# Kernel optimization log

Measured on AMD Instinct MI355X. Metric: run time of the kernel, lower is better.

## Reference

```python
import jax, jax.numpy as jnp
import numpy as np

IN_CH, OUT_CH, M1, M2 = 64, 64, 32, 32


def _powerlaw_psd_gaussian(key, exponent, n):
    """JAX port of colorednoise.powerlaw_psd_gaussian (fmin=0 default)."""
    f = jnp.fft.rfftfreq(n).astype(jnp.float32)  # [n//2+1]
    # fmin = max(0, 1/n); f[0]=0 is the only freq below it -> clamp to f[1]
    s_scale = jnp.where(f < 1.0 / n, f[1], f) ** (-exponent / 2.0)
    w = s_scale[1:]
    w = w.at[-1].multiply((1 + (n % 2)) / 2.0)  # Nyquist correction
    sigma = 2.0 * jnp.sqrt(jnp.sum(w * w)) / n
    kr, ki = jax.random.split(key)
    sr = jax.random.normal(kr, f.shape, jnp.float32) * s_scale
    si = jax.random.normal(ki, f.shape, jnp.float32) * s_scale
    if n % 2 == 0:
        si = si.at[-1].set(0.0)
        sr = sr.at[-1].multiply(jnp.sqrt(2.0))
    si = si.at[0].set(0.0)
    sr = sr.at[0].multiply(jnp.sqrt(2.0))
    return jnp.fft.irfft(sr + 1j * si, n=n) / sigma


def _compl_mul2d(t1, w, e_r, e_i, amp_r, amp_i, phi_r, phi_i, key):
    # Faithful to the torch code: stack over in-ch at dim=1 then sum dim=2
    # sums over the OUT channel axis => out[b,i,x,y] = t1[b,i,x,y]*sum_o w[i,o,x,y]
    out = t1 * jnp.sum(w, axis=1)[None]  # [B, IN_CH, M1, M2] complex
    b, c, m1, m2 = out.shape
    n = b * c * m1 * m2
    k1, k2 = jax.random.split(key)
    nr = jnp.roll(_powerlaw_psd_gaussian(k1, e_r, n), phi_r.astype(jnp.int32)) * amp_r
    ni = jnp.roll(_powerlaw_psd_gaussian(k2, e_i, n), phi_i.astype(jnp.int32)) * amp_i
    # original multiplies imag noise by amp_i twice (once in-place, once on reshape)
    noise = (nr + 1j * (ni * amp_i)).reshape(b, c, m1, m2)
    return out - noise


def _forward(x, w1, w2, exp_r, exp_i, nAmp_real, nAmp_imag, nPhase_real, nphase_imag):
    w1c = w1[..., 0] + 1j * w1[..., 1]  # [IN, OUT, M1, M2] complex64
    w2c = w2[..., 0] + 1j * w2[..., 1]
    e_r = jnp.median(exp_r)
    e_i = jnp.median(exp_i)
    amp_r = jnp.median(nAmp_real)
    amp_i = jnp.median(nAmp_imag)
    phi_r = jnp.median(nPhase_real)
    phi_i = jnp.median(nphase_imag)
    B, _, H, W = x.shape
    Wr = W // 2 + 1
    x_ft = jnp.fft.rfft2(x)  # [B, IN_CH, H, Wr]
    key = jax.random.key(42)
    kA, kB = jax.random.split(key)
    out_ft = jnp.zeros((B, OUT_CH, H, Wr), jnp.complex64)
    out_ft = out_ft.at[:, :, :M1, :M2].set(
        _compl_mul2d(x_ft[:, :, :M1, :M2], w1c, e_r, e_i, amp_r, amp_i, phi_r, phi_i, kA))
    out_ft = out_ft.at[:, :, -M1:, :M2].set(
        _compl_mul2d(x_ft[:, :, -M1:, :M2], w2c, e_r, e_i, amp_r, amp_i, phi_r, phi_i, kB))
    return jnp.fft.irfft2(out_ft, s=(H, W)).astype(jnp.float32)


def setup_inputs() -> dict:
    key = jax.random.key(0)
    ks = jax.random.split(key, 9)
    scale = 1.0 / (IN_CH * OUT_CH)
    return {
        "x": jax.random.normal(ks[0], (16, IN_CH, 256, 256), jnp.float32),
        "w1": scale * jax.random.uniform(ks[1], (IN_CH, OUT_CH, M1, M2, 2), jnp.float32),
        "w2": scale * jax.random.uniform(ks[2], (IN_CH, OUT_CH, M1, M2, 2), jnp.float32),
        "exp_r": jax.random.uniform(ks[3], (8,), jnp.float32),
        "exp_i": jax.random.uniform(ks[4], (8,), jnp.float32),
        "nAmp_real": jax.random.uniform(ks[5], (8,), jnp.float32),
        "nAmp_imag": jax.random.uniform(ks[6], (8,), jnp.float32),
        "nPhase_real": jax.random.normal(ks[7], (8,), jnp.float32),
        "nphase_imag": jax.random.normal(ks[8], (8,), jnp.float32),
    }


def reference(x, w1, w2, exp_r, exp_i, nAmp_real, nAmp_imag, nPhase_real, nphase_imag):
    return _forward(x, w1, w2, exp_r, exp_i, nAmp_real, nAmp_imag, nPhase_real, nphase_imag)
```

## Files before the change

kernel.cpp:

```cpp
#include <hip/hip_runtime.h>
#include <cstdint>

#define JPART 1
#define PART_XOR 1

constexpr uint32_t N20   = 1u << 20;
constexpr uint32_t NHALF = 1u << 19;
constexpr int SPT_STRIDE = 520;

struct Hdr {
  float e_r, e_i, amp_r, amp_i;
  int   phi_r, phi_i;
  float nhe_r, nhe_i;
  float scale_s[4];
};
struct KeyArgs { uint32_t k[8][2]; };

typedef __attribute__((ext_vector_type(8))) short short8;
typedef __attribute__((ext_vector_type(16))) float f32x16;

__device__ inline f32x16 zero16() {
  f32x16 v;
  #pragma unroll
  for (int i = 0; i < 16; ++i) v[i] = 0.f;
  return v;
}

__device__ inline unsigned short f2bf(float f) {
  uint32_t u = __float_as_uint(f);
  return (unsigned short)((u + 0x7fffu + ((u >> 16) & 1u)) >> 16);
}

__host__ __device__ inline void tf2x32(uint32_t k0, uint32_t k1, uint32_t x0, uint32_t x1,
                                       uint32_t& o0, uint32_t& o1) {
  const uint32_t ks0 = k0, ks1 = k1, ks2 = k0 ^ k1 ^ 0x1BD11BDAu;
  const uint32_t ks[3] = { ks0, ks1, ks2 };
  x0 += ks0; x1 += ks1;
  const int rot[2][4] = { {13,15,26,6}, {17,29,16,24} };
  for (int g = 0; g < 5; ++g) {
    const int* rr = rot[g & 1];
    for (int i = 0; i < 4; ++i) {
      x0 += x1;
      x1 = (x1 << rr[i]) | (x1 >> (32 - rr[i]));
      x1 ^= x0;
    }
    x0 += ks[(g + 1) % 3];
    x1 += ks[(g + 2) % 3] + (uint32_t)(g + 1);
  }
  o0 = x0; o1 = x1;
}

__device__ inline float erfinv_xla(float x) {
  float w = -log1pf(-x * x);
  float p;
  if (w < 5.0f) {
    w -= 2.5f;
    p = 2.81022636e-08f;
    p = fmaf(p, w, 3.43273939e-07f);
    p = fmaf(p, w, -3.5233877e-06f);
    p = fmaf(p, w, -4.39150654e-06f);
    p = fmaf(p, w, 0.00021858087f);
    p = fmaf(p, w, -0.00125372503f);
    p = fmaf(p, w, -0.00417768164f);
    p = fmaf(p, w, 0.246640727f);
    p = fmaf(p, w, 1.50140941f);
  } else {
    w = sqrtf(w) - 3.0f;
    p = -0.000200214257f;
    p = fmaf(p, w, 0.000100950558f);
    p = fmaf(p, w, 0.00134934322f);
    p = fmaf(p, w, -0.00367342844f);
    p = fmaf(p, w, 0.00573950773f);
    p = fmaf(p, w, -0.0076224613f);
    p = fmaf(p, w, 0.00943887047f);
    p = fmaf(p, w, 1.00167406f);
    p = fmaf(p, w, 2.83297682f);
  }
  return p * x;
}

__device__ inline float normal_from_bits(uint32_t bits) {
  uint32_t fb = (bits >> 9) | 0x3f800000u;
  float f = __uint_as_float(fb) - 1.0f;
  const float LO = -0.99999994f;
  float u = f * 2.0f + LO;
  u = fmaxf(LO, u);
  return 1.41421356f * erfinv_xla(u);
}

__device__ inline float sscale_f(uint32_t k, float nhe) {
  uint32_t kk = k ? k : 1u;
  return powf((float)kk * (1.0f / 1048576.0f), nhe);
}

__device__ inline float2 cmul(float2 a, float2 b) {
  return make_float2(a.x * b.x - a.y * b.y, a.x * b.y + a.y * b.x);
}
__device__ inline float2 wexp(float u) {
  float s, c; sincospif(2.0f * u, &s, &c); return make_float2(c, s);
}
__device__ inline float2 cadd(float2 a, float2 b){ return make_float2(a.x+b.x, a.y+b.y); }
__device__ inline float2 csub(float2 a, float2 b){ return make_float2(a.x-b.x, a.y-b.y); }
__device__ inline float2 cmuli(float2 a){ return make_float2(-a.y, a.x); }

__device__ inline int sA(int p) { return p ^ (((p >> 6) & 3) << 2) ^ ((p >> 8) & 3); }

__device__ inline void bfly(float2& y0, float2& y1, float2& y2, float2& y3, float2 W) {
  float2 a = cadd(y0, y2), b = csub(y0, y2);
  float2 c = cadd(y1, y3), d = cmuli(csub(y1, y3));
  float2 W2 = cmul(W, W), W3 = cmul(W2, W);
  y0 = cadd(a, c);
  y1 = cmul(cadd(b, d), W);
  y2 = cmul(csub(a, c), W2);
  y3 = cmul(csub(b, d), W3);
}

__device__ inline void fft1024_core(float2* r, float2* rc, float2* buf, int w) {
  #pragma unroll
  for (int e3 = 0; e3 < 4; ++e3) {
    float2 W = wexp((float)((e3 << 6) + w) * (1.0f / 1024.0f));
    bfly(r[e3], r[e3 + 4], r[e3 + 8], r[e3 + 12], W);
  }
  {
    float2 W = wexp((float)w * (1.0f / 256.0f));
    #pragma unroll
    for (int e4 = 0; e4 < 4; ++e4)
      bfly(r[(e4 << 2) + 0], r[(e4 << 2) + 1], r[(e4 << 2) + 2], r[(e4 << 2) + 3], W);
  }
  #pragma unroll
  for (int s = 0; s < 16; ++s) buf[sA((s << 6) + w)] = r[s];
  __syncthreads();
  {
    const int e0 = w & 3;
    const int pbase = ((w >> 4) << 8) + (((w >> 2) & 3) << 6) + e0;
    float2 rb[16];
    #pragma unroll
    for (int e2 = 0; e2 < 4; ++e2)
      #pragma unroll
      for (int e1 = 0; e1 < 4; ++e1)
        rb[(e2 << 2) + e1] = buf[sA(pbase + (e2 << 4) + (e1 << 2))];
    #pragma unroll
    for (int e1 = 0; e1 < 4; ++e1) {
      float2 W = wexp((float)((e1 << 2) + e0) * (1.0f / 64.0f));
      bfly(rb[e1], rb[e1 + 4], rb[e1 + 8], rb[e1 + 12], W);
    }
    {
      float2 W = wexp((float)e0 * (1.0f / 16.0f));
      #pragma unroll
      for (int e2 = 0; e2 < 4; ++e2)
        bfly(rb[(e2 << 2) + 0], rb[(e2 << 2) + 1], rb[(e2 << 2) + 2], rb[(e2 << 2) + 3], W);
    }
    #pragma unroll
    for (int e2 = 0; e2 < 4; ++e2)
      #pragma unroll
      for (int e1 = 0; e1 < 4; ++e1)
        buf[sA(pbase + (e2 << 4) + (e1 << 2))] = rb[(e2 << 2) + e1];
  }
  __syncthreads();
  {
    const int cbase = ((w >> 4) << 8) + (((w >> 2) & 3) << 6) + ((w & 3) << 4);
    #pragma unroll
    for (int e1 = 0; e1 < 4; ++e1)
      #pragma unroll
      for (int e0 = 0; e0 < 4; ++e0)
        rc[(e1 << 2) + e0] = buf[sA(cbase + (e1 << 2) + e0)];
    #pragma unroll
    for (int e1 = 0; e1 < 4; ++e1) {
      float2 x0 = rc[(e1 << 2)], x1 = rc[(e1 << 2) + 1], x2 = rc[(e1 << 2) + 2], x3 = rc[(e1 << 2) + 3];
      float2 a = cadd(x0, x2), b = csub(x0, x2);
      float2 c = cadd(x1, x3), d = cmuli(csub(x1, x3));
      rc[(e1 << 2)]     = cadd(a, c);
      rc[(e1 << 2) + 1] = cadd(b, d);
      rc[(e1 << 2) + 2] = csub(a, c);
      rc[(e1 << 2) + 3] = csub(b, d);
    }
  }
}

__device__ inline float med8_dev(const float* p) {
  float v[8];
  for (int i = 0; i < 8; ++i) v[i] = p[i];
  for (int i = 1; i < 8; ++i) { float key = v[i]; int j = i - 1;
    while (j >= 0 && v[j] > key) { v[j + 1] = v[j]; --j; } v[j + 1] = key; }
  return 0.5f * (v[3] + v[4]);
}

__global__ void k_scalars(Hdr* h, const float* er, const float* ei, const float* ar,
                          const float* ai, const float* pr, const float* pim) {
  if (threadIdx.x || blockIdx.x) return;
  float mer = med8_dev(er), mei = med8_dev(ei);
  h->e_r = mer; h->e_i = mei;
  h->amp_r = med8_dev(ar); h->amp_i = med8_dev(ai);
  h->phi_r = (int)med8_dev(pr);
  h->phi_i = (int)med8_dev(pim);
  h->nhe_r = -0.5f * mer; h->nhe_i = -0.5f * mei;
}

__global__ void k_sumw2(const Hdr* __restrict__ h, float* __restrict__ partials) {
  __shared__ float sr_[256], si_[256];
  const float nher = h->nhe_r, nhei = h->nhe_i;
  float sr = 0.f, si = 0.f;
  for (int j = 0; j < 4; ++j) {
    uint32_t k = (uint32_t)(blockIdx.x * 1024 + j * 256 + threadIdx.x) + 1u;
    float fk = (float)k * (1.0f / 1048576.0f);
    float wr = powf(fk, nher), wi = powf(fk, nhei);
    if (k == NHALF) { wr *= 0.5f; wi *= 0.5f; }
    sr += wr * wr; si += wi * wi;
  }
  sr_[threadIdx.x] = sr; si_[threadIdx.x] = si; __syncthreads();
  for (int off = 128; off > 0; off >>= 1) {
    if ((int)threadIdx.x < off) { sr_[threadIdx.x] += sr_[threadIdx.x + off];
                                  si_[threadIdx.x] += si_[threadIdx.x + off]; }
    __syncthreads();
  }
  if (!threadIdx.x) { partials[blockIdx.x * 2] = sr_[0]; partials[blockIdx.x * 2 + 1] = si_[0]; }
}

__global__ void k_sumw2_fin(Hdr* h, const float* partials) {
  if (threadIdx.x || blockIdx.x) return;
  float Sr = 0.f, Si = 0.f;
  for (int b = 0; b < 512; ++b) { Sr += partials[b * 2]; Si += partials[b * 2 + 1]; }
  float sig_r = 2.0f * sqrtf(Sr) * (1.0f / 1048576.0f);
  float sig_i = 2.0f * sqrtf(Si) * (1.0f / 1048576.0f);
  float s0 = h->amp_r / (sig_r * 1048576.0f);
  float s1 = (h->amp_i * h->amp_i) / (sig_i * 1048576.0f);
  h->scale_s[0] = s0; h->scale_s[1] = s1; h->scale_s[2] = s0; h->scale_s[3] = s1;
}

__global__ void k_wsum(const float* __restrict__ w1, const float* __restrict__ w2,
                       float2* __restrict__ wsum) {
  int idx = blockIdx.x * 256 + threadIdx.x;
  int sel = idx >> 16, rem = idx & 65535;
  const float* w = sel ? w2 : w1;
  int c = rem >> 10, m1 = (rem >> 5) & 31, m2 = rem & 31;
  size_t base = (size_t)c * 131072 + (size_t)m1 * 64 + (size_t)m2 * 2;
  float sr = 0.f, si = 0.f;
  for (int oc = 0; oc < 64; ++oc) { sr += w[base + (size_t)oc * 2048]; si += w[base + (size_t)oc * 2048 + 1]; }
  wsum[idx] = make_float2(sr, si);
}

__global__ void k_noise_spec(float4* __restrict__ spT, const Hdr* __restrict__ h, KeyArgs ka) {
  const int pair = blockIdx.y;
  const int bx = blockIdx.x;
  const int k1 = bx >> 1, chunk = bx & 1;
  const int k2 = (chunk << 8) + (int)threadIdx.x;
  const float nher = h->nhe_r, nhei = h->nhe_i;
  float4* row = spT + (size_t)pair * (1024 * SPT_STRIDE) + (size_t)k1 * SPT_STRIDE;
  const bool extra = (k1 == 0) && (chunk == 1) && (threadIdx.x == 255);
  const int niter = extra ? 2 : 1;
  for (int it = 0; it < niter; ++it) {
    const int kk2 = (it == 0) ? k2 : 512;
    const uint32_t i = (uint32_t)k1 + ((uint32_t)kk2 << 10);
    float vals[4];
    #pragma unroll
    for (int j = 0; j < 4; ++j) {
      const uint32_t K0 = ka.k[pair * 4 + j][0], K1 = ka.k[pair * 4 + j][1];
      uint32_t o0, o1; tf2x32(K0, K1, 0u, i, o0, o1);
#if PART_XOR
      uint32_t bits = o0 ^ o1;
#else
      uint32_t bits = o1;
#endif
      float nhe = (j < 2) ? nher : nhei;
      float v = normal_from_bits(bits) * sscale_f(i, nhe);
      if (i == 0u || i == NHALF) v = (j & 1) ? 0.0f : v * 1.41421356f;
      vals[j] = v;
    }
    row[kk2] = make_float4(vals[0], vals[1], vals[2], vals[3]);
  }
}

__global__ __launch_bounds__(256) void k_fft_s1(const float4* __restrict__ spT,
                                                float2* __restrict__ G) {
  __shared__ float2 buf4[4][1024];
  const int b = blockIdx.x;
  const int lin = (b & 7) * 64 + (b >> 3);
  const int pair = lin >> 8;
  const int g = threadIdx.x >> 6, w = threadIdx.x & 63;
  const int k1 = ((lin & 255) << 2) + g;
  const float4* sp = spT + (size_t)pair * (1024 * SPT_STRIDE);
  const int mrow = (1024 - k1) & 1023;

  float2 r[16], rc[16];
  #pragma unroll
  for (int s = 0; s < 16; ++s) {
    int k2 = (s << 6) + w;
    uint32_t k = (uint32_t)k1 + ((uint32_t)k2 << 10);
    float4 f; float2 z;
    if (k <= NHALF) {
      f = sp[(size_t)k1 * SPT_STRIDE + k2];
      z = make_float2(f.x - f.w, f.y + f.z);
    } else {
      int k2p = (k1 == 0) ? (1024 - k2) : (1023 - k2);
      f = sp[(size_t)mrow * SPT_STRIDE + k2p];
      z = make_float2(f.x + f.w, f.z - f.y);
    }
    r[s] = z;
  }
  fft1024_core(r, rc, buf4[g], w);
  float2* gp = G + ((size_t)pair << 20) + ((size_t)k1 << 10);
  const int klo = ((w & 3) << 4) + (((w >> 2) & 3) << 2) + (w >> 4);
  #pragma unroll
  for (int e1 = 0; e1 < 4; ++e1)
    #pragma unroll
    for (int e0 = 0; e0 < 4; ++e0) {
      int k = (e0 << 8) + (e1 << 6) + klo;
      float2 tw = wexp((float)(k * k1) * (1.0f / 1048576.0f));
      gp[k] = cmul(rc[(e1 << 2) + e0], tw);
    }
}

__global__ __launch_bounds__(256) void k_fft_s2(const float2* __restrict__ G,
                                                float2* __restrict__ noiseP,
                                                const Hdr* __restrict__ h) {
  __shared__ float2 buf4[4][1024];
  const int b = blockIdx.x;
  const int lin = (b & 7) * 64 + (b >> 3);
  const int pair = lin >> 8;
  const int g = threadIdx.x >> 6, w = threadIdx.x & 63;
  const int j2 = ((lin & 255) << 2) + g;

  float2 r[16], rc[16];
  const float2* gp = G + ((size_t)pair << 20) + (size_t)j2;
  #pragma unroll
  for (int s = 0; s < 16; ++s) r[s] = gp[(size_t)((s << 6) + w) << 10];
  fft1024_core(r, rc, buf4[g], w);
  const float scr = h->scale_s[0], sci = h->scale_s[1];
  float2* np_ = noiseP + ((size_t)pair << 20) + ((size_t)j2 << 10);
  const int klo = ((w & 3) << 4) + (((w >> 2) & 3) << 2) + (w >> 4);
  #pragma unroll
  for (int e1 = 0; e1 < 4; ++e1)
    #pragma unroll
    for (int e0 = 0; e0 < 4; ++e0) {
      int k = (e0 << 8) + (e1 << 6) + klo;
      np_[k] = make_float2(rc[(e1 << 2) + e0].x * scr, rc[(e1 << 2) + e0].y * sci);
    }
}

__global__ __launch_bounds__(256) void k_ntrans(const float2* __restrict__ noiseP,
                                                float* __restrict__ noiseL,
                                                const Hdr* __restrict__ h) {
  __shared__ float tr[64][65];
  __shared__ float ti[64][65];
  const int b = blockIdx.x;
  const int pair = b >> 8, tid = b & 255;
  const int R0 = (tid >> 4) << 6;
  const int C0 = (tid & 15) << 6;
  const int t = threadIdx.x;
  const int tx = t & 63, ty = t >> 6;
  const int phir = h->phi_r, phii = h->phi_i;
  const float2* src = noiseP + ((size_t)pair << 20);
  float* dstr = noiseL + ((size_t)(pair * 2) << 20);
  float* dsti = noiseL + ((size_t)(pair * 2 + 1) << 20);
  #pragma unroll
  for (int i = 0; i < 16; ++i) {
    int r = (i << 2) + ty;
    float2 v = src[(size_t)((R0 + r) << 10) + (size_t)(C0 + tx)];
    tr[r][tx] = v.x; ti[r][tx] = v.y;
  }
  __syncthreads();
  #pragma unroll
  for (int i = 0; i < 16; ++i) {
    int c = (i << 2) + ty;
    int n = ((C0 + c) << 10) + R0 + tx;
    dstr[(uint32_t)(n + phir) & (N20 - 1u)] = tr[tx][c];
    dsti[(uint32_t)(n + phii) & (N20 - 1u)] = ti[tx][c];
  }
}

__global__ __launch_bounds__(256) void k_prep(unsigned short* __restrict__ A_E,
                                              unsigned short* __restrict__ B2T,
                                              unsigned short* __restrict__ ET,
                                              unsigned short* __restrict__ Fc,
                                              unsigned short* __restrict__ Fs,
                                              unsigned short* __restrict__ Fns) {
  int t = blockIdx.x * 256 + threadIdx.x;
  if (t < 32768) {
    int y = t >> 7, p = t & 127;
    int kyp = p & 63; int ky = (kyp < 32) ? kyp : kyp + 192;
    float s, c; sincospif(2.0f * (float)((ky * y) & 255) * (1.0f / 256.0f), &s, &c);
    A_E[t] = f2bf((p < 64) ? c : s);
  } else if (t < 49152) {
    int u = t - 32768;
    int x = u >> 6, j = u & 63, kx = j & 31;
    float s, c; sincospif(2.0f * (float)((kx * x) & 255) * (1.0f / 256.0f), &s, &c);
    float v = (j < 32) ? ((kx == 0) ? 1.0f : 2.0f * c)
                       : ((kx == 0) ? 0.0f : -2.0f * s);
    B2T[u] = f2bf(v * (1.0f / 65536.0f));
  } else if (t < 65536) {
    int u = t - 49152;
    int col = u >> 8, xx = u & 255; int kx = col & 31;
    float s, c; sincospif(2.0f * (float)((kx * xx) & 255) * (1.0f / 256.0f), &s, &c);
    ET[u] = f2bf((col < 32) ? c : -s);
  } else if (t < 114688) {
    int u = (t - 65536) & 16383;
    int which = (t - 65536) >> 14;
    int kyp = u >> 8, y = u & 255; int ky = (kyp < 32) ? kyp : kyp + 192;
    float s, c; sincospif(2.0f * (float)((ky * y) & 255) * (1.0f / 256.0f), &s, &c);
    if (which == 0) Fc[u] = f2bf(c);
    else if (which == 1) Fs[u] = f2bf(s);
    else Fns[u] = f2bf(-s);
  }
}

__global__ __launch_bounds__(256, 2) void k_forward(const float* __restrict__ x,
    const float2* __restrict__ wsum, const float* __restrict__ noiseL,
    const unsigned short* __restrict__ ET, const unsigned short* __restrict__ Fc,
    const unsigned short* __restrict__ Fs, const unsigned short* __restrict__ Fns,
    float2* __restrict__ oftg) {
  __shared__ char lds[65536];
  char* X1T = lds + 32768;
  const int bc = blockIdx.x, t = threadIdx.x;
  const int c = bc & 63;
  const int l = t & 63, w = t >> 6, lr = l & 31, kg = l >> 5;
  const int rt = w >> 1, ct = w & 1;
  const float* xim = x + ((size_t)bc << 16);

  const int r_  = t >> 2;
  (void)r_;
  float4 pf[16];
  #pragma unroll
  for (int i = 0; i < 16; ++i) {
    int f4 = i * 256 + t;
    int r = f4 >> 6, c4 = f4 & 63;
    pf[i] = *(const float4*)(xim + (size_t)((r) << 8) + (c4 << 2));
  }

  #pragma unroll
  for (int yt = 0; yt < 4; ++yt) {
    __syncthreads();
    #pragma unroll
    for (int i = 0; i < 16; ++i) {
      int f4 = i * 256 + t;
      int r = f4 >> 6, c4 = f4 & 63;
      ushort4 b4; b4.x = f2bf(pf[i].x); b4.y = f2bf(pf[i].y);
      b4.z = f2bf(pf[i].z); b4.w = f2bf(pf[i].w);
      int byte = ((r << 9) + (c4 << 3)) ^ ((r & 7) << 4);
      *(ushort4*)(lds + byte) = b4;
    }
    __syncthreads();
    if (yt < 3) {
      #pragma unroll
      for (int i = 0; i < 16; ++i) {
        int f4 = i * 256 + t;
        int r = f4 >> 6, c4 = f4 & 63;
        pf[i] = *(const float4*)(xim + (size_t)((((yt + 1) << 6) + r) << 8) + (c4 << 2));
      }
    }
    f32x16 a1 = zero16();
    const int arow = (rt << 5) + lr;
    const int bcol = (ct << 5) + lr;
    #pragma unroll
    for (int s = 0; s < 16; ++s) {
      short8 af = *(const short8*)(lds + (((arow << 9) + (s << 5) + (kg << 4)) ^ ((arow & 7) << 4)));
      short8 bf = *(const short8*)(ET + (bcol << 8) + (s << 4) + (kg << 3));
      a1 = __builtin_amdgcn_mfma_f32_32x32x16_bf16(af, bf, a1, 0, 0, 0);
    }
    #pragma unroll
    for (int r4 = 0; r4 < 4; ++r4) {
      int y0 = (yt << 6) + (rt << 5) + (r4 << 3) + (kg << 2);
      ushort4 p4;
      p4.x = f2bf(a1[r4 * 4 + 0]); p4.y = f2bf(a1[r4 * 4 + 1]);
      p4.z = f2bf(a1[r4 * 4 + 2]); p4.w = f2bf(a1[r4 * 4 + 3]);
      int byte = ((bcol << 9) + (y0 << 1)) ^ ((bcol & 7) << 4);
      *(ushort4*)(X1T + byte) = p4;
    }
  }
  __syncthreads();

  const int re_im = w >> 1, kt = w & 1;
  const unsigned short* A1p = re_im ? Fns : Fs;
  const int b0row = (re_im ? 32 : 0) + lr;
  const int b1row = (re_im ? 0 : 32) + lr;
  const int a2row = (kt << 5) + lr;
  f32x16 a2 = zero16();
  #pragma unroll
  for (int s = 0; s < 16; ++s) {
    short8 a0f = *(const short8*)(Fc  + (a2row << 8) + (s << 4) + (kg << 3));
    short8 a1f = *(const short8*)(A1p + (a2row << 8) + (s << 4) + (kg << 3));
    short8 b0f = *(const short8*)(X1T + (((b0row << 9) + (s << 5) + (kg << 4)) ^ ((b0row & 7) << 4)));
    short8 b1f = *(const short8*)(X1T + (((b1row << 9) + (s << 5) + (kg << 4)) ^ ((b1row & 7) << 4)));
    a2 = __builtin_amdgcn_mfma_f32_32x32x16_bf16(a0f, b0f, a2, 0, 0, 0);
    a2 = __builtin_amdgcn_mfma_f32_32x32x16_bf16(a1f, b1f, a2, 0, 0, 0);
  }
  float* Osm = (float*)(lds + (re_im << 13));
  #pragma unroll
  for (int i = 0; i < 16; ++i) {
    int row = (kt << 5) + (i & 3) + ((i >> 2) << 3) + (kg << 2);
    Osm[(row << 5) + lr] = a2[i];
  }
  __syncthreads();

  const float* Ore = (const float*)lds;
  const float* Oim = (const float*)(lds + 8192);
  #pragma unroll
  for (int r = 0; r < 8; ++r) {
    int idx = (r << 8) + t;
    int kyp = idx >> 5, kx = idx & 31;
    int sel = kyp >> 5, m1 = kyp & 31;
    float2 av = make_float2(Ore[idx], Oim[idx]);
    float2 wv = wsum[((size_t)sel << 16) + (size_t)(((c << 5) | m1) << 5) + (size_t)kx];
    float2 v;
    v.x = av.x * wv.x - av.y * wv.y;
    v.y = av.x * wv.y + av.y * wv.x;
    uint32_t p = ((uint32_t)((bc << 5) | m1) << 5) | (uint32_t)kx;
    const float* nlr = noiseL + ((size_t)(sel ? 2 : 0) << 20);
    const float* nli = noiseL + ((size_t)(sel ? 3 : 1) << 20);
    v.x -= nlr[p];
    v.y -= nli[p];
    oftg[((size_t)bc << 11) + (size_t)idx] = v;
  }
}

__global__ __launch_bounds__(256) void k_inverse(const float2* __restrict__ oftg,
    const unsigned short* __restrict__ A_E, const unsigned short* __restrict__ B2T,
    float* __restrict__ out) {
  __shared__ char smem[49152];
  char* Tb = smem + 16384;
  float* ofs = (float*)(smem + 16384);

  const int bc = blockIdx.x, t = threadIdx.x;
  const int l = t & 63, w = t >> 6, lr = l & 31, kg = l >> 5;

  {
    const float4* src = (const float4*)(oftg + ((size_t)bc << 11));
    float4* dst = (float4*)ofs;
    #pragma unroll
    for (int i = 0; i < 4; ++i) dst[t + (i << 8)] = src[t + (i << 8)];
  }
  __syncthreads();

  #pragma unroll
  for (int i = 0; i < 32; ++i) {
    int idx = t + (i << 8);
    int p = idx >> 6, j = idx & 63;
    int kyp = p & 63;
    float v;
    if (p < 64) v = (j < 32) ? ofs[(kyp << 6) + (j << 1)]
                             : ofs[(kyp << 6) + ((j - 32) << 1) + 1];
    else        v = (j < 32) ? -ofs[(kyp << 6) + (j << 1) + 1]
                             : ofs[(kyp << 6) + ((j - 32) << 1)];
    int byte = ((j << 8) + (p << 1)) ^ ((j & 7) << 4);
    *(unsigned short*)(smem + byte) = f2bf(v);
  }
  __syncthreads();

  f32x16 acc[2][2];
  acc[0][0] = zero16(); acc[0][1] = zero16(); acc[1][0] = zero16(); acc[1][1] = zero16();
  #pragma unroll
  for (int s = 0; s < 8; ++s) {
    short8 af[2], bf[2];
    #pragma unroll
    for (int rt = 0; rt < 2; ++rt) {
      int row = (w << 6) + (rt << 5) + lr;
      af[rt] = *(const short8*)(A_E + (row << 7) + (s << 4) + (kg << 3));
    }
    #pragma unroll
    for (int ct = 0; ct < 2; ++ct) {
      int j = (ct << 5) + lr;
      int byte = ((j << 8) + (s << 5) + (kg << 4)) ^ ((j & 7) << 4);
      bf[ct] = *(const short8*)(smem + byte);
    }
    #pragma unroll
    for (int rt = 0; rt < 2; ++rt)
      #pragma unroll
      for (int ct = 0; ct < 2; ++ct)
        acc[rt][ct] = __builtin_amdgcn_mfma_f32_32x32x16_bf16(af[rt], bf[ct], acc[rt][ct], 0, 0, 0);
  }

  #pragma unroll
  for (int rt = 0; rt < 2; ++rt)
    #pragma unroll
    for (int ct = 0; ct < 2; ++ct)
      #pragma unroll
      for (int r = 0; r < 16; ++r) {
        int row = (w << 6) + (rt << 5) + (r & 3) + (((r >> 2) & 3) << 3) + (kg << 2);
        int col = (ct << 5) + lr;
        int byte = ((row << 7) + (col << 1)) ^ ((row & 7) << 4);
        *(unsigned short*)(Tb + byte) = f2bf(acc[rt][ct][r]);
      }
  __syncthreads();

  short8 ta[2][4];
  #pragma unroll
  for (int rt = 0; rt < 2; ++rt)
    #pragma unroll
    for (int ks = 0; ks < 4; ++ks) {
      int row = (w << 6) + (rt << 5) + lr;
      int byte = ((row << 7) + (ks << 5) + (kg << 4)) ^ ((row & 7) << 4);
      ta[rt][ks] = *(const short8*)(Tb + byte);
    }
  float* op = out + ((size_t)bc << 16);
  #pragma unroll
  for (int cc = 0; cc < 4; ++cc) {
    short8 b2[2][4];
    #pragma unroll
    for (int cx = 0; cx < 2; ++cx)
      #pragma unroll
      for (int ks = 0; ks < 4; ++ks) {
        int xx = (cc << 6) + (cx << 5) + lr;
        b2[cx][ks] = *(const short8*)(B2T + (xx << 6) + (ks << 4) + (kg << 3));
      }
    f32x16 a2[2][2];
    a2[0][0] = zero16(); a2[0][1] = zero16(); a2[1][0] = zero16(); a2[1][1] = zero16();
    #pragma unroll
    for (int ks = 0; ks < 4; ++ks)
      #pragma unroll
      for (int rt = 0; rt < 2; ++rt)
        #pragma unroll
        for (int cx = 0; cx < 2; ++cx)
          a2[rt][cx] = __builtin_amdgcn_mfma_f32_32x32x16_bf16(ta[rt][ks], b2[cx][ks], a2[rt][cx], 0, 0, 0);
    #pragma unroll
    for (int rt = 0; rt < 2; ++rt)
      #pragma unroll
      for (int cx = 0; cx < 2; ++cx)
        #pragma unroll
        for (int r = 0; r < 16; ++r) {
          int row = (w << 6) + (rt << 5) + (r & 3) + (((r >> 2) & 3) << 3) + (kg << 2);
          int xx = (cc << 6) + (cx << 5) + lr;
          op[(row << 8) + xx] = a2[rt][cx][r];
        }
  }
}

extern "C" void kernel_launch(void* const* d_in, const int* in_sizes, int n_in,
                              void* d_out, int out_size, void* d_ws, size_t ws_size,
                              hipStream_t stream) {
  (void)in_sizes; (void)n_in; (void)out_size; (void)ws_size;
  const float* x   = (const float*)d_in[0];
  const float* w1  = (const float*)d_in[1];
  const float* w2  = (const float*)d_in[2];
  const float* er  = (const float*)d_in[3];
  const float* ei  = (const float*)d_in[4];
  const float* ar  = (const float*)d_in[5];
  const float* ai  = (const float*)d_in[6];
  const float* pr  = (const float*)d_in[7];
  const float* pim = (const float*)d_in[8];
  float* out = (float*)d_out;

  char* ws = (char*)d_ws;
  Hdr*    hdr      = (Hdr*)ws;
  float*  partials = (float*)(ws + 0x1000);
  float2* wsum     = (float2*)(ws + 0x10000);
  unsigned short* A_E = (unsigned short*)(ws + 0x130000);
  unsigned short* B2T = (unsigned short*)(ws + 0x140000);
  unsigned short* ET  = (unsigned short*)(ws + 0x148000);
  unsigned short* Fc  = (unsigned short*)(ws + 0x150000);
  unsigned short* Fs  = (unsigned short*)(ws + 0x158000);
  unsigned short* Fns = (unsigned short*)(ws + 0x160000);
  float4* spT      = (float4*)(ws + 0x200000);
  float2* G        = (float2*)(ws + 0x1400000);
  float2* oft      = (float2*)(ws + 0x1400000);
  float2* noiseP   = (float2*)(ws + 0x2400000);
  float*  noiseL   = (float*)(ws + 0x3400000);

  auto splitk = [](const uint32_t k[2], uint32_t a[2], uint32_t b[2]) {
#if JPART
    tf2x32(k[0], k[1], 0u, 0u, a[0], a[1]);
    tf2x32(k[0], k[1], 0u, 1u, b[0], b[1]);
#else
    uint32_t r0[2], r1[2];
    tf2x32(k[0], k[1], 0u, 2u, r0[0], r0[1]);
    tf2x32(k[0], k[1], 1u, 3u, r1[0], r1[1]);
    a[0] = r0[0]; a[1] = r1[0]; b[0] = r0[1]; b[1] = r1[1];
#endif
  };
  uint32_t root[2] = { 0u, 42u };
  uint32_t kA[2], kB[2], k1A[2], k2A[2], k1B[2], k2B[2];
  splitk(root, kA, kB);
  splitk(kA, k1A, k2A);
  splitk(kB, k1B, k2B);
  KeyArgs ka;
  splitk(k1A, ka.k[0], ka.k[1]);
  splitk(k2A, ka.k[2], ka.k[3]);
  splitk(k1B, ka.k[4], ka.k[5]);
  splitk(k2B, ka.k[6], ka.k[7]);

  hipLaunchKernelGGL(k_scalars,    dim3(1),        dim3(64),  0, stream, hdr, er, ei, ar, ai, pr, pim);
  hipLaunchKernelGGL(k_sumw2,      dim3(512),      dim3(256), 0, stream, hdr, partials);
  hipLaunchKernelGGL(k_sumw2_fin,  dim3(1),        dim3(64),  0, stream, hdr, partials);
  hipLaunchKernelGGL(k_wsum,       dim3(512),      dim3(256), 0, stream, w1, w2, wsum);
  hipLaunchKernelGGL(k_prep,       dim3(448),      dim3(256), 0, stream, A_E, B2T, ET, Fc, Fs, Fns);
  hipLaunchKernelGGL(k_noise_spec, dim3(2048, 2),  dim3(256), 0, stream, spT, hdr, ka);
  hipLaunchKernelGGL(k_fft_s1,     dim3(512),      dim3(256), 0, stream, spT, G);
  hipLaunchKernelGGL(k_fft_s2,     dim3(512),      dim3(256), 0, stream, G, noiseP, hdr);
  hipLaunchKernelGGL(k_ntrans,     dim3(512),      dim3(256), 0, stream, noiseP, noiseL, hdr);
  hipLaunchKernelGGL(k_forward,    dim3(1024),     dim3(256), 0, stream, x, wsum, noiseL, ET, Fc, Fs, Fns, oft);
  hipLaunchKernelGGL(k_inverse,    dim3(1024),     dim3(256), 0, stream, oft, A_E, B2T, out);
}
```

Measured before the change: 270.7 us.

## Merge small setup kernels into combined launches and shrink inverse-kernel shared memory

Folds the scalar medians, weight summation and basis prep into one k_misc launch, and the sum-of-squares reduction plus noise spectrum generation into one k_gen launch. This cuts the launch count from eleven to eight and lets independent small jobs share the GPU. k_inverse now reads oft straight from global memory instead of staging it in LDS, and reuses one 32KB buffer with an extra barrier. The aim is lower launch overhead and higher occupancy from the smaller LDS footprint, at the cost of uncoalesced global gathers in k_inverse.

After: 267.8 us. Within noise of the previous version (-1.1%).

```diff
diff --git a/kernel.cpp b/kernel.cpp
--- a/kernel.cpp
+++ b/kernel.cpp
@@ -185,196 +185,37 @@
   return 0.5f * (v[3] + v[4]);
 }
 
-__global__ void k_scalars(Hdr* h, const float* er, const float* ei, const float* ar,
-                          const float* ai, const float* pr, const float* pim) {
-  if (threadIdx.x || blockIdx.x) return;
-  float mer = med8_dev(er), mei = med8_dev(ei);
-  h->e_r = mer; h->e_i = mei;
-  h->amp_r = med8_dev(ar); h->amp_i = med8_dev(ai);
-  h->phi_r = (int)med8_dev(pr);
-  h->phi_i = (int)med8_dev(pim);
-  h->nhe_r = -0.5f * mer; h->nhe_i = -0.5f * mei;
-}
-
-__global__ void k_sumw2(const Hdr* __restrict__ h, float* __restrict__ partials) {
-  __shared__ float sr_[256], si_[256];
-  const float nher = h->nhe_r, nhei = h->nhe_i;
-  float sr = 0.f, si = 0.f;
-  for (int j = 0; j < 4; ++j) {
-    uint32_t k = (uint32_t)(blockIdx.x * 1024 + j * 256 + threadIdx.x) + 1u;
-    float fk = (float)k * (1.0f / 1048576.0f);
-    float wr = powf(fk, nher), wi = powf(fk, nhei);
-    if (k == NHALF) { wr *= 0.5f; wi *= 0.5f; }
-    sr += wr * wr; si += wi * wi;
-  }
-  sr_[threadIdx.x] = sr; si_[threadIdx.x] = si; __syncthreads();
-  for (int off = 128; off > 0; off >>= 1) {
-    if ((int)threadIdx.x < off) { sr_[threadIdx.x] += sr_[threadIdx.x + off];
-                                  si_[threadIdx.x] += si_[threadIdx.x + off]; }
-    __syncthreads();
-  }
-  if (!threadIdx.x) { partials[blockIdx.x * 2] = sr_[0]; partials[blockIdx.x * 2 + 1] = si_[0]; }
-}
-
-__global__ void k_sumw2_fin(Hdr* h, const float* partials) {
-  if (threadIdx.x || blockIdx.x) return;
-  float Sr = 0.f, Si = 0.f;
-  for (int b = 0; b < 512; ++b) { Sr += partials[b * 2]; Si += partials[b * 2 + 1]; }
-  float sig_r = 2.0f * sqrtf(Sr) * (1.0f / 1048576.0f);
-  float sig_i = 2.0f * sqrtf(Si) * (1.0f / 1048576.0f);
-  float s0 = h->amp_r / (sig_r * 1048576.0f);
-  float s1 = (h->amp_i * h->amp_i) / (sig_i * 1048576.0f);
-  h->scale_s[0] = s0; h->scale_s[1] = s1; h->scale_s[2] = s0; h->scale_s[3] = s1;
-}
-
-__global__ void k_wsum(const float* __restrict__ w1, const float* __restrict__ w2,
-                       float2* __restrict__ wsum) {
-  int idx = blockIdx.x * 256 + threadIdx.x;
-  int sel = idx >> 16, rem = idx & 65535;
-  const float* w = sel ? w2 : w1;
-  int c = rem >> 10, m1 = (rem >> 5) & 31, m2 = rem & 31;
-  size_t base = (size_t)c * 131072 + (size_t)m1 * 64 + (size_t)m2 * 2;
-  float sr = 0.f, si = 0.f;
-  for (int oc = 0; oc < 64; ++oc) { sr += w[base + (size_t)oc * 2048]; si += w[base + (size_t)oc * 2048 + 1]; }
-  wsum[idx] = make_float2(sr, si);
-}
-
-__global__ void k_noise_spec(float4* __restrict__ spT, const Hdr* __restrict__ h, KeyArgs ka) {
-  const int pair = blockIdx.y;
-  const int bx = blockIdx.x;
-  const int k1 = bx >> 1, chunk = bx & 1;
-  const int k2 = (chunk << 8) + (int)threadIdx.x;
-  const float nher = h->nhe_r, nhei = h->nhe_i;
-  float4* row = spT + (size_t)pair * (1024 * SPT_STRIDE) + (size_t)k1 * SPT_STRIDE;
-  const bool extra = (k1 == 0) && (chunk == 1) && (threadIdx.x == 255);
-  const int niter = extra ? 2 : 1;
-  for (int it = 0; it < niter; ++it) {
-    const int kk2 = (it == 0) ? k2 : 512;
-    const uint32_t i = (uint32_t)k1 + ((uint32_t)kk2 << 10);
-    float vals[4];
-    #pragma unroll
-    for (int j = 0; j < 4; ++j) {
-      const uint32_t K0 = ka.k[pair * 4 + j][0], K1 = ka.k[pair * 4 + j][1];
-      uint32_t o0, o1; tf2x32(K0, K1, 0u, i, o0, o1);
-#if PART_XOR
-      uint32_t bits = o0 ^ o1;
-#else
-      uint32_t bits = o1;
-#endif
-      float nhe = (j < 2) ? nher : nhei;
-      float v = normal_from_bits(bits) * sscale_f(i, nhe);
-      if (i == 0u || i == NHALF) v = (j & 1) ? 0.0f : v * 1.41421356f;
-      vals[j] = v;
-    }
-    row[kk2] = make_float4(vals[0], vals[1], vals[2], vals[3]);
-  }
-}
-
-__global__ __launch_bounds__(256) void k_fft_s1(const float4* __restrict__ spT,
-                                                float2* __restrict__ G) {
-  __shared__ float2 buf4[4][1024];
+__global__ __launch_bounds__(256) void k_misc(Hdr* h,
+    const float* er, const float* ei, const float* ar, const float* ai,
+    const float* pr, const float* pim,
+    const float* __restrict__ w1, const float* __restrict__ w2,
+    float2* __restrict__ wsum,
+    unsigned short* __restrict__ A_E, unsigned short* __restrict__ B2T,
+    unsigned short* __restrict__ ET, unsigned short* __restrict__ Fc,
+    unsigned short* __restrict__ Fs, unsigned short* __restrict__ Fns) {
   const int b = blockIdx.x;
-  const int lin = (b & 7) * 64 + (b >> 3);
-  const int pair = lin >> 8;
-  const int g = threadIdx.x >> 6, w = threadIdx.x & 63;
-  const int k1 = ((lin & 255) << 2) + g;
-  const float4* sp = spT + (size_t)pair * (1024 * SPT_STRIDE);
-  const int mrow = (1024 - k1) & 1023;
-
-  float2 r[16], rc[16];
-  #pragma unroll
-  for (int s = 0; s < 16; ++s) {
-    int k2 = (s << 6) + w;
-    uint32_t k = (uint32_t)k1 + ((uint32_t)k2 << 10);
-    float4 f; float2 z;
-    if (k <= NHALF) {
-      f = sp[(size_t)k1 * SPT_STRIDE + k2];
-      z = make_float2(f.x - f.w, f.y + f.z);
-    } else {
-      int k2p = (k1 == 0) ? (1024 - k2) : (1023 - k2);
-      f = sp[(size_t)mrow * SPT_STRIDE + k2p];
-      z = make_float2(f.x + f.w, f.z - f.y);
-    }
-    r[s] = z;
-  }
-  fft1024_core(r, rc, buf4[g], w);
-  float2* gp = G + ((size_t)pair << 20) + ((size_t)k1 << 10);
-  const int klo = ((w & 3) << 4) + (((w >> 2) & 3) << 2) + (w >> 4);
-  #pragma unroll
-  for (int e1 = 0; e1 < 4; ++e1)
-    #pragma unroll
-    for (int e0 = 0; e0 < 4; ++e0) {
-      int k = (e0 << 8) + (e1 << 6) + klo;
-      float2 tw = wexp((float)(k * k1) * (1.0f / 1048576.0f));
-      gp[k] = cmul(rc[(e1 << 2) + e0], tw);
-    }
-}
-
-__global__ __launch_bounds__(256) void k_fft_s2(const float2* __restrict__ G,
-                                                float2* __restrict__ noiseP,
-                                                const Hdr* __restrict__ h) {
-  __shared__ float2 buf4[4][1024];
-  const int b = blockIdx.x;
-  const int lin = (b & 7) * 64 + (b >> 3);
-  const int pair = lin >> 8;
-  const int g = threadIdx.x >> 6, w = threadIdx.x & 63;
-  const int j2 = ((lin & 255) << 2) + g;
-
-  float2 r[16], rc[16];
-  const float2* gp = G + ((size_t)pair << 20) + (size_t)j2;
-  #pragma unroll
-  for (int s = 0; s < 16; ++s) r[s] = gp[(size_t)((s << 6) + w) << 10];
-  fft1024_core(r, rc, buf4[g], w);
-  const float scr = h->scale_s[0], sci = h->scale_s[1];
-  float2* np_ = noiseP + ((size_t)pair << 20) + ((size_t)j2 << 10);
-  const int klo = ((w & 3) << 4) + (((w >> 2) & 3) << 2) + (w >> 4);
-  #pragma unroll
-  for (int e1 = 0; e1 < 4; ++e1)
-    #pragma unroll
-    for (int e0 = 0; e0 < 4; ++e0) {
-      int k = (e0 << 8) + (e1 << 6) + klo;
-      np_[k] = make_float2(rc[(e1 << 2) + e0].x * scr, rc[(e1 << 2) + e0].y * sci);
-    }
-}
-
-__global__ __launch_bounds__(256) void k_ntrans(const float2* __restrict__ noiseP,
-                                                float* __restrict__ noiseL,
-                                                const Hdr* __restrict__ h) {
-  __shared__ float tr[64][65];
-  __shared__ float ti[64][65];
-  const int b = blockIdx.x;
-  const int pair = b >> 8, tid = b & 255;
-  const int R0 = (tid >> 4) << 6;
-  const int C0 = (tid & 15) << 6;
-  const int t = threadIdx.x;
-  const int tx = t & 63, ty = t >> 6;
-  const int phir = h->phi_r, phii = h->phi_i;
-  const float2* src = noiseP + ((size_t)pair << 20);
-  float* dstr = noiseL + ((size_t)(pair * 2) << 20);
-  float* dsti = noiseL + ((size_t)(pair * 2 + 1) << 20);
-  #pragma unroll
-  for (int i = 0; i < 16; ++i) {
-    int r = (i << 2) + ty;
-    float2 v = src[(size_t)((R0 + r) << 10) + (size_t)(C0 + tx)];
-    tr[r][tx] = v.x; ti[r][tx] = v.y;
-  }
-  __syncthreads();
-  #pragma unroll
-  for (int i = 0; i < 16; ++i) {
-    int c = (i << 2) + ty;
-    int n = ((C0 + c) << 10) + R0 + tx;
-    dstr[(uint32_t)(n + phir) & (N20 - 1u)] = tr[tx][c];
-    dsti[(uint32_t)(n + phii) & (N20 - 1u)] = ti[tx][c];
-  }
-}
-
-__global__ __launch_bounds__(256) void k_prep(unsigned short* __restrict__ A_E,
-                                              unsigned short* __restrict__ B2T,
-                                              unsigned short* __restrict__ ET,
-                                              unsigned short* __restrict__ Fc,
-                                              unsigned short* __restrict__ Fs,
-                                              unsigned short* __restrict__ Fns) {
-  int t = blockIdx.x * 256 + threadIdx.x;
+  if (b == 960) {
+    if (threadIdx.x) return;
+    float mer = med8_dev(er), mei = med8_dev(ei);
+    h->e_r = mer; h->e_i = mei;
+    h->amp_r = med8_dev(ar); h->amp_i = med8_dev(ai);
+    h->phi_r = (int)med8_dev(pr);
+    h->phi_i = (int)med8_dev(pim);
+    h->nhe_r = -0.5f * mer; h->nhe_i = -0.5f * mei;
+    return;
+  }
+  if (b < 512) {
+    int idx = b * 256 + threadIdx.x;
+    int sel = idx >> 16, rem = idx & 65535;
+    const float* w = sel ? w2 : w1;
+    int c = rem >> 10, m1 = (rem >> 5) & 31, m2 = rem & 31;
+    size_t base = (size_t)c * 131072 + (size_t)m1 * 64 + (size_t)m2 * 2;
+    float sr = 0.f, si = 0.f;
+    for (int oc = 0; oc < 64; ++oc) { sr += w[base + (size_t)oc * 2048]; si += w[base + (size_t)oc * 2048 + 1]; }
+    wsum[idx] = make_float2(sr, si);
+    return;
+  }
+  int t = (b - 512) * 256 + threadIdx.x;
   if (t < 32768) {
     int y = t >> 7, p = t & 127;
     int kyp = p & 63; int ky = (kyp < 32) ? kyp : kyp + 192;
@@ -403,6 +244,170 @@
   }
 }
 
+__global__ __launch_bounds__(256) void k_gen(const Hdr* __restrict__ h,
+                                             float* __restrict__ partials,
+                                             float4* __restrict__ spT, KeyArgs ka) {
+  __shared__ float sr_[256], si_[256];
+  const int b = blockIdx.x;
+  if (b < 512) {
+    const float nher = h->nhe_r, nhei = h->nhe_i;
+    float sr = 0.f, si = 0.f;
+    for (int j = 0; j < 4; ++j) {
+      uint32_t k = (uint32_t)(b * 1024 + j * 256 + threadIdx.x) + 1u;
+      float fk = (float)k * (1.0f / 1048576.0f);
+      float wr = powf(fk, nher), wi = powf(fk, nhei);
+      if (k == NHALF) { wr *= 0.5f; wi *= 0.5f; }
+      sr += wr * wr; si += wi * wi;
+    }
+    sr_[threadIdx.x] = sr; si_[threadIdx.x] = si; __syncthreads();
+    for (int off = 128; off > 0; off >>= 1) {
+      if ((int)threadIdx.x < off) { sr_[threadIdx.x] += sr_[threadIdx.x + off];
+                                    si_[threadIdx.x] += si_[threadIdx.x + off]; }
+      __syncthreads();
+    }
+    if (!threadIdx.x) { partials[b * 2] = sr_[0]; partials[b * 2 + 1] = si_[0]; }
+    return;
+  }
+  const int idx = b - 512;
+  const int pair = idx >> 11;
+  const int bx = idx & 2047;
+  const int k1 = bx >> 1, chunk = bx & 1;
+  const int k2 = (chunk << 8) + (int)threadIdx.x;
+  const float nher = h->nhe_r, nhei = h->nhe_i;
+  float4* row = spT + (size_t)pair * (1024 * SPT_STRIDE) + (size_t)k1 * SPT_STRIDE;
+  const bool extra = (k1 == 0) && (chunk == 1) && (threadIdx.x == 255);
+  const int niter = extra ? 2 : 1;
+  for (int it = 0; it < niter; ++it) {
+    const int kk2 = (it == 0) ? k2 : 512;
+    const uint32_t i = (uint32_t)k1 + ((uint32_t)kk2 << 10);
+    float vals[4];
+    #pragma unroll
+    for (int j = 0; j < 4; ++j) {
+      const uint32_t K0 = ka.k[pair * 4 + j][0], K1 = ka.k[pair * 4 + j][1];
+      uint32_t o0, o1; tf2x32(K0, K1, 0u, i, o0, o1);
+#if PART_XOR
+      uint32_t bits = o0 ^ o1;
+#else
+      uint32_t bits = o1;
+#endif
+      float nhe = (j < 2) ? nher : nhei;
+      float v = normal_from_bits(bits) * sscale_f(i, nhe);
+      if (i == 0u || i == NHALF) v = (j & 1) ? 0.0f : v * 1.41421356f;
+      vals[j] = v;
+    }
+    row[kk2] = make_float4(vals[0], vals[1], vals[2], vals[3]);
+  }
+}
+
+__global__ void k_sumw2_fin(Hdr* h, const float* partials) {
+  if (threadIdx.x || blockIdx.x) return;
+  float Sr = 0.f, Si = 0.f;
+  for (int b = 0; b < 512; ++b) { Sr += partials[b * 2]; Si += partials[b * 2 + 1]; }
+  float sig_r = 2.0f * sqrtf(Sr) * (1.0f / 1048576.0f);
+  float sig_i = 2.0f * sqrtf(Si) * (1.0f / 1048576.0f);
+  float s0 = h->amp_r / (sig_r * 1048576.0f);
+  float s1 = (h->amp_i * h->amp_i) / (sig_i * 1048576.0f);
+  h->scale_s[0] = s0; h->scale_s[1] = s1; h->scale_s[2] = s0; h->scale_s[3] = s1;
+}
+
+__global__ __launch_bounds__(256) void k_fft_s1(const float4* __restrict__ spT,
+                                                float2* __restrict__ G) {
+  __shared__ float2 buf4[4][1024];
+  const int b = blockIdx.x;
+  const int lin = (b & 7) * 64 + (b >> 3);
+  const int pair = lin >> 8;
+  const int g = threadIdx.x >> 6, w = threadIdx.x & 63;
+  const int k1 = ((lin & 255) << 2) + g;
+  const float4* sp = spT + (size_t)pair * (1024 * SPT_STRIDE);
+  const int mrow = (1024 - k1) & 1023;
+
+  float2 r[16], rc[16];
+  #pragma unroll
+  for (int s = 0; s < 16; ++s) {
+    int k2 = (s << 6) + w;
+    uint32_t k = (uint32_t)k1 + ((uint32_t)k2 << 10);
+    float4 f; float2 z;
+    if (k <= NHALF) {
+      f = sp[(size_t)k1 * SPT_STRIDE + k2];
+      z = make_float2(f.x - f.w, f.y + f.z);
+    } else {
+      int k2p = (k1 == 0) ? (1024 - k2) : (1023 - k2);
+      f = sp[(size_t)mrow * SPT_STRIDE + k2p];
+      z = make_float2(f.x + f.w, f.z - f.y);
+    }
+    r[s] = z;
+  }
+  fft1024_core(r, rc, buf4[g], w);
+  float2* gp = G + ((size_t)pair << 20) + ((size_t)k1 << 10);
+  const int klo = ((w & 3) << 4) + (((w >> 2) & 3) << 2) + (w >> 4);
+  #pragma unroll
+  for (int e1 = 0; e1 < 4; ++e1)
+    #pragma unroll
+    for (int e0 = 0; e0 < 4; ++e0) {
+      int k = (e0 << 8) + (e1 << 6) + klo;
+      float2 tw = wexp((float)(k * k1) * (1.0f / 1048576.0f));
+      gp[k] = cmul(rc[(e1 << 2) + e0], tw);
+    }
+}
+
+__global__ __launch_bounds__(256) void k_fft_s2(const float2* __restrict__ G,
+                                                float2* __restrict__ noiseP,
+                                                const Hdr* __restrict__ h) {
+  __shared__ float2 buf4[4][1024];
+  const int b = blockIdx.x;
+  const int lin = (b & 7) * 64 + (b >> 3);
+  const int pair = lin >> 8;
+  const int g = threadIdx.x >> 6, w = threadIdx.x & 63;
+  const int j2 = ((lin & 255) << 2) + g;
+
+  float2 r[16], rc[16];
+  const float2* gp = G + ((size_t)pair << 20) + (size_t)j2;
+  #pragma unroll
+  for (int s = 0; s < 16; ++s) r[s] = gp[(size_t)((s << 6) + w) << 10];
+  fft1024_core(r, rc, buf4[g], w);
+  const float scr = h->scale_s[0], sci = h->scale_s[1];
+  float2* np_ = noiseP + ((size_t)pair << 20) + ((size_t)j2 << 10);
+  const int klo = ((w & 3) << 4) + (((w >> 2) & 3) << 2) + (w >> 4);
+  #pragma unroll
+  for (int e1 = 0; e1 < 4; ++e1)
+    #pragma unroll
+    for (int e0 = 0; e0 < 4; ++e0) {
+      int k = (e0 << 8) + (e1 << 6) + klo;
+      np_[k] = make_float2(rc[(e1 << 2) + e0].x * scr, rc[(e1 << 2) + e0].y * sci);
+    }
+}
+
+__global__ __launch_bounds__(256) void k_ntrans(const float2* __restrict__ noiseP,
+                                                float* __restrict__ noiseL,
+                                                const Hdr* __restrict__ h) {
+  __shared__ float tr[64][65];
+  __shared__ float ti[64][65];
+  const int b = blockIdx.x;
+  const int pair = b >> 8, tid = b & 255;
+  const int R0 = (tid >> 4) << 6;
+  const int C0 = (tid & 15) << 6;
+  const int t = threadIdx.x;
+  const int tx = t & 63, ty = t >> 6;
+  const int phir = h->phi_r, phii = h->phi_i;
+  const float2* src = noiseP + ((size_t)pair << 20);
+  float* dstr = noiseL + ((size_t)(pair * 2) << 20);
+  float* dsti = noiseL + ((size_t)(pair * 2 + 1) << 20);
+  #pragma unroll
+  for (int i = 0; i < 16; ++i) {
+    int r = (i << 2) + ty;
+    float2 v = src[(size_t)((R0 + r) << 10) + (size_t)(C0 + tx)];
+    tr[r][tx] = v.x; ti[r][tx] = v.y;
+  }
+  __syncthreads();
+  #pragma unroll
+  for (int i = 0; i < 16; ++i) {
+    int c = (i << 2) + ty;
+    int n = ((C0 + c) << 10) + R0 + tx;
+    dstr[(uint32_t)(n + phir) & (N20 - 1u)] = tr[tx][c];
+    dsti[(uint32_t)(n + phii) & (N20 - 1u)] = ti[tx][c];
+  }
+}
+
 __global__ __launch_bounds__(256, 2) void k_forward(const float* __restrict__ x,
     const float2* __restrict__ wsum, const float* __restrict__ noiseL,
     const unsigned short* __restrict__ ET, const unsigned short* __restrict__ Fc,
@@ -416,8 +421,6 @@
   const int rt = w >> 1, ct = w & 1;
   const float* xim = x + ((size_t)bc << 16);
 
-  const int r_  = t >> 2;
-  (void)r_;
   float4 pf[16];
   #pragma unroll
   for (int i = 0; i < 16; ++i) {
@@ -515,33 +518,26 @@
 __global__ __launch_bounds__(256) void k_inverse(const float2* __restrict__ oftg,
     const unsigned short* __restrict__ A_E, const unsigned short* __restrict__ B2T,
     float* __restrict__ out) {
-  __shared__ char smem[49152];
-  char* Tb = smem + 16384;
-  float* ofs = (float*)(smem + 16384);
+  __shared__ char smem[32768];
 
   const int bc = blockIdx.x, t = threadIdx.x;
   const int l = t & 63, w = t >> 6, lr = l & 31, kg = l >> 5;
 
   {
-    const float4* src = (const float4*)(oftg + ((size_t)bc << 11));
-    float4* dst = (float4*)ofs;
-    #pragma unroll
-    for (int i = 0; i < 4; ++i) dst[t + (i << 8)] = src[t + (i << 8)];
-  }
-  __syncthreads();
-
-  #pragma unroll
-  for (int i = 0; i < 32; ++i) {
-    int idx = t + (i << 8);
-    int p = idx >> 6, j = idx & 63;
-    int kyp = p & 63;
-    float v;
-    if (p < 64) v = (j < 32) ? ofs[(kyp << 6) + (j << 1)]
-                             : ofs[(kyp << 6) + ((j - 32) << 1) + 1];
-    else        v = (j < 32) ? -ofs[(kyp << 6) + (j << 1) + 1]
-                             : ofs[(kyp << 6) + ((j - 32) << 1)];
-    int byte = ((j << 8) + (p << 1)) ^ ((j & 7) << 4);
-    *(unsigned short*)(smem + byte) = f2bf(v);
+    const float* ob = (const float*)(oftg + ((size_t)bc << 11));
+    #pragma unroll
+    for (int i = 0; i < 32; ++i) {
+      int idx = t + (i << 8);
+      int p = idx >> 6, j = idx & 63;
+      int kyp = p & 63;
+      float v;
+      if (p < 64) v = (j < 32) ? ob[(kyp << 6) + (j << 1)]
+                               : ob[(kyp << 6) + ((j - 32) << 1) + 1];
+      else        v = (j < 32) ? -ob[(kyp << 6) + (j << 1) + 1]
+                               : ob[(kyp << 6) + ((j - 32) << 1)];
+      int byte = ((j << 8) + (p << 1)) ^ ((j & 7) << 4);
+      *(unsigned short*)(smem + byte) = f2bf(v);
+    }
   }
   __syncthreads();
 
@@ -567,6 +563,7 @@
       for (int ct = 0; ct < 2; ++ct)
         acc[rt][ct] = __builtin_amdgcn_mfma_f32_32x32x16_bf16(af[rt], bf[ct], acc[rt][ct], 0, 0, 0);
   }
+  __syncthreads();
 
   #pragma unroll
   for (int rt = 0; rt < 2; ++rt)
@@ -577,7 +574,7 @@
         int row = (w << 6) + (rt << 5) + (r & 3) + (((r >> 2) & 3) << 3) + (kg << 2);
         int col = (ct << 5) + lr;
         int byte = ((row << 7) + (col << 1)) ^ ((row & 7) << 4);
-        *(unsigned short*)(Tb + byte) = f2bf(acc[rt][ct][r]);
+        *(unsigned short*)(smem + byte) = f2bf(acc[rt][ct][r]);
       }
   __syncthreads();
 
@@ -588,7 +585,7 @@
     for (int ks = 0; ks < 4; ++ks) {
       int row = (w << 6) + (rt << 5) + lr;
       int byte = ((row << 7) + (ks << 5) + (kg << 4)) ^ ((row & 7) << 4);
-      ta[rt][ks] = *(const short8*)(Tb + byte);
+      ta[rt][ks] = *(const short8*)(smem + byte);
     }
   float* op = out + ((size_t)bc << 16);
   #pragma unroll
@@ -676,15 +673,13 @@
   splitk(k1B, ka.k[4], ka.k[5]);
   splitk(k2B, ka.k[6], ka.k[7]);
 
-  hipLaunchKernelGGL(k_scalars,    dim3(1),        dim3(64),  0, stream, hdr, er, ei, ar, ai, pr, pim);
-  hipLaunchKernelGGL(k_sumw2,      dim3(512),      dim3(256), 0, stream, hdr, partials);
-  hipLaunchKernelGGL(k_sumw2_fin,  dim3(1),        dim3(64),  0, stream, hdr, partials);
-  hipLaunchKernelGGL(k_wsum,       dim3(512),      dim3(256), 0, stream, w1, w2, wsum);
-  hipLaunchKernelGGL(k_prep,       dim3(448),      dim3(256), 0, stream, A_E, B2T, ET, Fc, Fs, Fns);
-  hipLaunchKernelGGL(k_noise_spec, dim3(2048, 2),  dim3(256), 0, stream, spT, hdr, ka);
-  hipLaunchKernelGGL(k_fft_s1,     dim3(512),      dim3(256), 0, stream, spT, G);
-  hipLaunchKernelGGL(k_fft_s2,     dim3(512),      dim3(256), 0, stream, G, noiseP, hdr);
-  hipLaunchKernelGGL(k_ntrans,     dim3(512),      dim3(256), 0, stream, noiseP, noiseL, hdr);
-  hipLaunchKernelGGL(k_forward,    dim3(1024),     dim3(256), 0, stream, x, wsum, noiseL, ET, Fc, Fs, Fns, oft);
-  hipLaunchKernelGGL(k_inverse,    dim3(1024),     dim3(256), 0, stream, oft, A_E, B2T, out);
-}
+  hipLaunchKernelGGL(k_misc,      dim3(961),      dim3(256), 0, stream, hdr, er, ei, ar, ai, pr, pim,
+                     w1, w2, wsum, A_E, B2T, ET, Fc, Fs, Fns);
+  hipLaunchKernelGGL(k_gen,       dim3(4608),     dim3(256), 0, stream, hdr, partials, spT, ka);
+  hipLaunchKernelGGL(k_sumw2_fin, dim3(1),        dim3(64),  0, stream, hdr, partials);
+  hipLaunchKernelGGL(k_fft_s1,    dim3(512),      dim3(256), 0, stream, spT, G);
+  hipLaunchKernelGGL(k_fft_s2,    dim3(512),      dim3(256), 0, stream, G, noiseP, hdr);
+  hipLaunchKernelGGL(k_ntrans,    dim3(512),      dim3(256), 0, stream, noiseP, noiseL, hdr);
+  hipLaunchKernelGGL(k_forward,   dim3(1024),     dim3(256), 0, stream, x, wsum, noiseL, ET, Fc, Fs, Fns, oft);
+  hipLaunchKernelGGL(k_inverse,   dim3(1024),     dim3(256), 0, stream, oft, A_E, B2T, out);
+}
```
